# Performance work log

Measured on AMD Instinct MI355X. Metric: run time of the kernel, lower is better.

The kernel has to match this reference:

```python
import jax, jax.numpy as jnp
import numpy as np

D_MODEL = 512
D_STATE = 32
EXPAND = 2
D_INNER = D_MODEL * EXPAND
BATCH = 2
SEQ_LEN = 1024


def setup_inputs() -> dict:
    key = jax.random.key(0)
    ks = jax.random.split(key, 8)
    s = lambda fan_in: 1.0 / np.sqrt(fan_in)
    x = jax.random.normal(ks[0], (BATCH, SEQ_LEN, D_MODEL), dtype=jnp.float32)
    Wx = jax.random.uniform(ks[1], (D_INNER, D_MODEL), minval=-s(D_MODEL), maxval=s(D_MODEL))
    Wdt = jax.random.uniform(ks[2], (D_INNER, D_MODEL), minval=-s(D_MODEL), maxval=s(D_MODEL))
    bdt = jax.random.uniform(ks[3], (D_INNER,)) + 1.0  # dt_proj.bias init: rand + 1
    A_log = jnp.log(jax.random.uniform(ks[4], (D_INNER, D_STATE), minval=1e-4, maxval=1.0))
    WB = jax.random.uniform(ks[5], (D_INNER * D_STATE, D_MODEL), minval=-s(D_MODEL), maxval=s(D_MODEL))
    WC = jax.random.uniform(ks[6], (D_INNER * D_STATE, D_MODEL), minval=-s(D_MODEL), maxval=s(D_MODEL))
    Wout = jax.random.uniform(ks[7], (D_MODEL, D_INNER), minval=-s(D_INNER), maxval=s(D_INNER))
    return {"x": x, "Wx": Wx, "Wdt": Wdt, "bdt": bdt, "A_log": A_log,
            "WB": WB, "WC": WC, "Wout": Wout}


def reference(x, Wx, Wdt, bdt, A_log, WB, WC, Wout):
    b, L, _ = x.shape
    d_inner, d_state = A_log.shape

    x_inner = jnp.einsum('bld,ed->ble', x, Wx)                 # (b, L, d_inner)
    delta = jax.nn.softplus(jnp.einsum('bld,ed->ble', x, Wdt) + bdt)
    A = -jnp.exp(A_log.astype(jnp.float32))                    # (d_inner, d_state)
    A_disc = jnp.exp(delta[..., None] * A)                     # (b, L, d_inner, d_state)
    Bm = jnp.einsum('bld,ed->ble', x, WB).reshape(b, L, d_inner, d_state)
    Cm = jnp.einsum('bld,ed->ble', x, WC).reshape(b, L, d_inner, d_state)

    def step(h, inp):
        a_t, b_t, c_t, x_t = inp
        h = a_t * h + b_t * x_t[..., None]                     # (b, d_inner, d_state)
        y = jnp.sum(c_t * h, axis=-1)                          # (b, d_inner)
        return h, y

    h0 = jnp.zeros((b, d_inner, d_state), dtype=x.dtype)
    xs = (jnp.moveaxis(A_disc, 1, 0), jnp.moveaxis(Bm, 1, 0),
          jnp.moveaxis(Cm, 1, 0), jnp.moveaxis(x_inner, 1, 0))
    _, ys = jax.lax.scan(step, h0, xs)                         # ys: (L, b, d_inner)
    y = jnp.moveaxis(ys, 0, 1)
    y = y * jax.nn.sigmoid(y)                                  # SiLU
    return jnp.einsum('ble,de->bld', y, Wout)
```

## Files before the change

### kernel.cpp

```cpp
#include <hip/hip_runtime.h>

#define BATCH   2
#define SEQLEN  1024
#define DMODEL  512
#define DSTATE  32
#define DINNER  1024
#define MROWS   (BATCH*SEQLEN)
#define NPROJ   (2*DINNER + 2*DINNER*DSTATE)

typedef short bf16x8 __attribute__((ext_vector_type(8)));
typedef float f32x4  __attribute__((ext_vector_type(4)));

__device__ __forceinline__ unsigned short f2bf(float f) {
    union { float f; unsigned u; } c; c.f = f;
    unsigned u = c.u;
    u += 0x7fffu + ((u >> 16) & 1u);
    return (unsigned short)(u >> 16);
}
__device__ __forceinline__ float bf2f(unsigned short h) {
    union { unsigned u; float f; } c; c.u = ((unsigned)h) << 16;
    return c.f;
}

__global__ void cast_all(const float4* __restrict__ Wx, const float4* __restrict__ Wdt,
                         const float4* __restrict__ WB, const float4* __restrict__ WC,
                         const float4* __restrict__ x,  const float4* __restrict__ Wout,
                         unsigned short* __restrict__ Wbf,
                         unsigned short* __restrict__ Xbf,
                         unsigned short* __restrict__ Woutbf) {
    const long nWx = 131072, nWdt = 131072, nWB = 4194304, nWC = 4194304;
    const long nWall = nWx + nWdt + nWB + nWC;
    const long nX = 262144, nWo = 131072;
    const long total = nWall + nX + nWo;
    for (long u = (long)blockIdx.x * blockDim.x + threadIdx.x; u < total;
         u += (long)gridDim.x * blockDim.x) {
        float4 v; unsigned short* dst;
        if (u < nWall) {
            if (u < nWx)             v = Wx[u];
            else if (u < nWx+nWdt)   v = Wdt[u - nWx];
            else if (u < nWx+nWdt+nWB) v = WB[u - nWx - nWdt];
            else                     v = WC[u - nWx - nWdt - nWB];
            dst = Wbf + u*4;
        } else if (u < nWall + nX) {
            v = x[u - nWall];       dst = Xbf + (u - nWall)*4;
        } else {
            v = Wout[u - nWall - nX]; dst = Woutbf + (u - nWall - nX)*4;
        }
        ushort4 o; o.x = f2bf(v.x); o.y = f2bf(v.y); o.z = f2bf(v.z); o.w = f2bf(v.w);
        *(ushort4*)dst = o;
    }
}

template<int EPI>
__global__ __launch_bounds__(256)
void gemm_bt(const unsigned short* __restrict__ A, const unsigned short* __restrict__ Bw,
             int K, int N, int t0, int Tchunk, int tgs,
             float* __restrict__ xin, float* __restrict__ dlt,
             unsigned short* __restrict__ Bout, unsigned short* __restrict__ Cout,
             const float* __restrict__ bdt, float* __restrict__ outf) {
    __shared__ unsigned short Asm[2][128*32];
    __shared__ unsigned short Bsm[2][128*32];
    const int tid  = threadIdx.x;
    const int w    = tid >> 6;
    const int lane = tid & 63;
    const int wm   = w >> 1, wn = w & 1;

    const int nx = gridDim.x, ny = gridDim.y;
    int ntile, rtile;
    if ((nx & 7) == 0) {
        const int lin = blockIdx.x + nx * blockIdx.y;
        const int xcd = lin & 7;
        const int sl  = lin >> 3;
        ntile = xcd * (nx >> 3) + sl / ny;
        rtile = sl % ny;
    } else {
        ntile = blockIdx.x; rtile = blockIdx.y;
    }

    const int rr0  = rtile * 128;
    const int bb   = (rr0 >= Tchunk) ? 1 : 0;
    const int grow0 = bb * SEQLEN + t0 + (rr0 - bb * Tchunk);
    const int n0   = ntile * 128;

    f32x4 acc[4][4] = {};

    const unsigned short* Ag = A  + (size_t)grow0 * K;
    const unsigned short* Bg = Bw + (size_t)n0 * K;

    const int c0 = w*64 + lane;
    const int c1 = c0 + 256;
    const int r   = lane & 15;
    const int h16 = lane >> 4;

    const int rowc0 = c0 >> 2, rowc1 = c1 >> 2;
    const int subc0 = (c0 & 3) ^ ((c0 >> 3) & 3);
    const int subc1 = (c1 & 3) ^ ((c1 >> 3) & 3);
    const size_t srcA0 = (size_t)rowc0 * K + subc0 * 8;
    const size_t srcA1 = (size_t)rowc1 * K + subc1 * 8;

    const int nt = K >> 5;

    #define STAGE(k0_, buf_)                                                              \
        do {                                                                              \
            __builtin_amdgcn_global_load_lds(                                             \
                (const __attribute__((address_space(1))) void*)(Ag + srcA0 + (k0_)),      \
                (__attribute__((address_space(3))) void*)(&Asm[(buf_)][w*512]), 16, 0, 0);\
            __builtin_amdgcn_global_load_lds(                                             \
                (const __attribute__((address_space(1))) void*)(Ag + srcA1 + (k0_)),      \
                (__attribute__((address_space(3))) void*)(&Asm[(buf_)][2048 + w*512]), 16, 0, 0); \
            __builtin_amdgcn_global_load_lds(                                             \
                (const __attribute__((address_space(1))) void*)(Bg + srcA0 + (k0_)),      \
                (__attribute__((address_space(3))) void*)(&Bsm[(buf_)][w*512]), 16, 0, 0);\
            __builtin_amdgcn_global_load_lds(                                             \
                (const __attribute__((address_space(1))) void*)(Bg + srcA1 + (k0_)),      \
                (__attribute__((address_space(3))) void*)(&Bsm[(buf_)][2048 + w*512]), 16, 0, 0); \
        } while (0)

    #define COMPUTE(buf_)                                                                 \
        do {                                                                              \
            bf16x8 af[4], bfr[4];                                                         \
            _Pragma("unroll")                                                             \
            for (int i = 0; i < 4; i++) {                                                 \
                const int Ra = wm*64 + i*16 + r;                                          \
                const int Rb = wn*64 + i*16 + r;                                          \
                af[i]  = *(const bf16x8*)(&Asm[(buf_)][Ra*32 + (h16 ^ ((Ra>>1)&3))*8]);   \
                bfr[i] = *(const bf16x8*)(&Bsm[(buf_)][Rb*32 + (h16 ^ ((Rb>>1)&3))*8]);   \
            }                                                                             \
            _Pragma("unroll")                                                             \
            for (int i = 0; i < 4; i++)                                                   \
                _Pragma("unroll")                                                         \
                for (int j = 0; j < 4; j++)                                               \
                    acc[i][j] = __builtin_amdgcn_mfma_f32_16x16x32_bf16(af[i], bfr[j], acc[i][j], 0, 0, 0); \
        } while (0)

    STAGE(0, 0);
    for (int it = 0; it < nt - 1; ++it) {
        const int cur = it & 1;
        STAGE((it + 1) * 32, cur ^ 1);
        asm volatile("s_waitcnt vmcnt(4)" ::: "memory");
        __builtin_amdgcn_s_barrier();
        COMPUTE(cur);
        asm volatile("" ::: "memory");
        __builtin_amdgcn_s_barrier();
        asm volatile("" ::: "memory");
    }
    asm volatile("s_waitcnt vmcnt(0)" ::: "memory");
    __builtin_amdgcn_s_barrier();
    COMPUTE((nt - 1) & 1);

    #undef STAGE
    #undef COMPUTE

    const int q = lane >> 4;
    const int Tg  = 1 << tgs;
    const int NT  = Tg >> 3;
    #pragma unroll
    for (int i = 0; i < 4; i++) {
        const int lr0 = wm*64 + i*16 + q*4;
        #pragma unroll
        for (int j = 0; j < 4; j++) {
            const int ncol = n0 + wn*64 + j*16 + r;
            if (EPI == 0) {
                const int cr   = rr0 + lr0;
                const int lt   = cr - bb*Tchunk;
                const int seg  = lt >> tgs;
                const int tloc = lt & (Tg - 1);
                const int kin  = tloc >> 3;
                const int tin  = tloc & 7;
                const int bs   = bb*8 + seg;
                if (ncol < 1024) {
                    float4 o = {acc[i][j][0], acc[i][j][1], acc[i][j][2], acc[i][j][3]};
                    *(float4*)(xin + ((size_t)bs*1024 + ncol)*Tg + tloc) = o;
                } else if (ncol < 2048) {
                    const float bias = bdt[ncol - 1024];
                    float4 o;
                    {   float z0 = acc[i][j][0] + bias; o.x = (z0 > 20.f) ? z0 : log1pf(__expf(z0));
                        float z1 = acc[i][j][1] + bias; o.y = (z1 > 20.f) ? z1 : log1pf(__expf(z1));
                        float z2 = acc[i][j][2] + bias; o.z = (z2 > 20.f) ? z2 : log1pf(__expf(z2));
                        float z3 = acc[i][j][3] + bias; o.w = (z3 > 20.f) ? z3 : log1pf(__expf(z3)); }
                    *(float4*)(dlt + ((size_t)bs*1024 + (ncol-1024))*Tg + tloc) = o;
                } else if (ncol < 34816) {
                    const int es = ncol - 2048;
                    short4 o;
                    o.x = (short)f2bf(acc[i][j][0]); o.y = (short)f2bf(acc[i][j][1]);
                    o.z = (short)f2bf(acc[i][j][2]); o.w = (short)f2bf(acc[i][j][3]);
                    *(short4*)(Bout + (((size_t)bs*1024 + (es>>5))*NT + kin)*256 + (es&31)*8 + tin) = o;
                } else {
                    const int es = ncol - 34816;
                    short4 o;
                    o.x = (short)f2bf(acc[i][j][0]); o.y = (short)f2bf(acc[i][j][1]);
                    o.z = (short)f2bf(acc[i][j][2]); o.w = (short)f2bf(acc[i][j][3]);
                    *(short4*)(Cout + (((size_t)bs*1024 + (es>>5))*NT + kin)*256 + (es&31)*8 + tin) = o;
                }
            } else {
                #pragma unroll
                for (int t = 0; t < 4; t++)
                    outf[(size_t)(grow0 + lr0 + t)*N + ncol] = acc[i][j][t];
            }
        }
    }
}

template<int NT>
__global__ __launch_bounds__(256)
void scan_fused(const float* __restrict__ dlt, const float* __restrict__ xin,
                const unsigned short* __restrict__ Bbf, const unsigned short* __restrict__ Cbf,
                const float* __restrict__ A_log,
                unsigned short* __restrict__ Ybf, float* __restrict__ hbuf,
                int t0, int first) {
    const int tid = threadIdx.x;
    const int g = tid >> 5, s = tid & 31;
    const int G = blockIdx.x;
    const int b = G >> 10, e = G & 1023;
    const int bs = b*8 + g;
    const int Tg = NT * 8;

    const float Aes = -__expf(A_log[e*32 + s]);

    const float* dp = dlt + ((size_t)bs*1024 + e)*Tg;
    const float* xp = xin + ((size_t)bs*1024 + e)*Tg;
    const unsigned short* bp = Bbf + ((size_t)bs*1024 + e)*NT*256 + s*8;
    const unsigned short* cp = Cbf + ((size_t)bs*1024 + e)*NT*256 + s*8;

    bf16x8 Bc[NT];
    #pragma unroll
    for (int k = 0; k < NT; k++) Bc[k] = *(const bf16x8*)(bp + (size_t)k*256);

    float h = 0.f, ap = 1.f;
    #pragma unroll
    for (int k = 0; k < NT; k++) {
        const float4 d0 = *(const float4*)(dp + k*8), d1 = *(const float4*)(dp + k*8 + 4);
        const float4 x0 = *(const float4*)(xp + k*8), x1 = *(const float4*)(xp + k*8 + 4);
        const float db[8] = {d0.x,d0.y,d0.z,d0.w,d1.x,d1.y,d1.z,d1.w};
        const float xb[8] = {x0.x,x0.y,x0.z,x0.w,x1.x,x1.y,x1.z,x1.w};
        #pragma unroll
        for (int j = 0; j < 8; j++) {
            const float a = __expf(db[j] * Aes);
            h = a*h + bf2f((unsigned short)Bc[k][j])*xb[j];
            ap *= a;
        }
    }

    __shared__ float Lh[8][32];
    __shared__ float La[8][32];
    Lh[g][s] = h; La[g][s] = ap;
    __syncthreads();
    float hin = first ? 0.f : hbuf[(size_t)G*32 + s];
    #pragma unroll
    for (int j = 0; j < 7; j++) {
        if (j < g) hin = La[j][s]*hin + Lh[j][s];
    }
    if (g == 7) hbuf[(size_t)G*32 + s] = La[7][s]*hin + Lh[7][s];

    h = hin;
    const int tbase = t0 + g*Tg;
    #pragma unroll
    for (int k = 0; k < NT; k++) {
        const bf16x8 cv = *(const bf16x8*)(cp + (size_t)k*256);
        const float4 d0 = *(const float4*)(dp + k*8), d1 = *(const float4*)(dp + k*8 + 4);
        const float4 x0 = *(const float4*)(xp + k*8), x1 = *(const float4*)(xp + k*8 + 4);
        const float db[8] = {d0.x,d0.y,d0.z,d0.w,d1.x,d1.y,d1.z,d1.w};
        const float xb[8] = {x0.x,x0.y,x0.z,x0.w,x1.x,x1.y,x1.z,x1.w};
        float p[8];
        #pragma unroll
        for (int j = 0; j < 8; j++) {
            const float a = __expf(db[j] * Aes);
            h = a*h + bf2f((unsigned short)Bc[k][j])*xb[j];
            p[j] = bf2f((unsigned short)cv[j])*h;
        }
        #pragma unroll
        for (int i2 = 0; i2 < 4; i2++) {
            float send = (s & 16) ? p[i2] : p[i2+4];
            float recv = __shfl_xor(send, 16, 32);
            p[i2] = ((s & 16) ? p[i2+4] : p[i2]) + recv;
        }
        #pragma unroll
        for (int i2 = 0; i2 < 2; i2++) {
            float send = (s & 8) ? p[i2] : p[i2+2];
            float recv = __shfl_xor(send, 8, 32);
            p[i2] = ((s & 8) ? p[i2+2] : p[i2]) + recv;
        }
        {
            float send = (s & 4) ? p[0] : p[1];
            float recv = __shfl_xor(send, 4, 32);
            p[0] = ((s & 4) ? p[1] : p[0]) + recv;
        }
        p[0] += __shfl_xor(p[0], 2, 32);
        p[0] += __shfl_xor(p[0], 1, 32);
        if ((s & 3) == 0) {
            const int tl = s >> 2;
            const float qv = p[0];
            const float y = qv * __builtin_amdgcn_rcpf(1.f + __expf(-qv));
            Ybf[(size_t)b*1048576 + e + (size_t)(tbase + k*8 + tl)*1024] = f2bf(y);
        }
    }
}

extern "C" void kernel_launch(void* const* d_in, const int* in_sizes, int n_in,
                              void* d_out, int out_size, void* d_ws, size_t ws_size,
                              hipStream_t stream) {
    const float* x     = (const float*)d_in[0];
    const float* Wx    = (const float*)d_in[1];
    const float* Wdt   = (const float*)d_in[2];
    const float* bdt   = (const float*)d_in[3];
    const float* A_log = (const float*)d_in[4];
    const float* WB    = (const float*)d_in[5];
    const float* WC    = (const float*)d_in[6];
    const float* Wout  = (const float*)d_in[7];

    char* ws = (char*)d_ws;
    unsigned short* Wbf    = (unsigned short*)(ws);
    unsigned short* Xbf    = (unsigned short*)(ws + 69206016);
    unsigned short* Woutbf = (unsigned short*)(ws + 71303168);
    float*          xin    = (float*)        (ws + 72351744);
    float*          dlt    = (float*)        (ws + 80740352);
    unsigned short* Ybf    = (unsigned short*)(ws + 89128960);
    float*          hbuf   = (float*)        (ws + 93323264);
    unsigned short* Bbf    = (unsigned short*)(ws + 99876864);
    const size_t fixedB = 99876864;

    int T = 128;
    const int cands[4] = {1024, 512, 256, 128};
    for (int ci = 0; ci < 4; ci++) {
        if (fixedB + (size_t)2 * cands[ci] * 131072 <= ws_size) { T = cands[ci]; break; }
    }
    unsigned short* Cbf = Bbf + (size_t)T * 65536;

    const int Tg = T / 8;
    int tgs = 0; while ((1 << tgs) < Tg) tgs++;
    const int NT = Tg / 8;

    cast_all<<<dim3(2048), dim3(256), 0, stream>>>(
        (const float4*)Wx, (const float4*)Wdt, (const float4*)WB, (const float4*)WC,
        (const float4*)x, (const float4*)Wout, Wbf, Xbf, Woutbf);

    const int NC = SEQLEN / T;
    for (int c = 0; c < NC; c++) {
        const int t0 = c * T;
        const int first = (c == 0) ? 1 : 0;
        gemm_bt<0><<<dim3(NPROJ/128, 2*T/128), dim3(256), 0, stream>>>(
            Xbf, Wbf, DMODEL, NPROJ, t0, T, tgs, xin, dlt, Bbf, Cbf, bdt, nullptr);
        if (NT == 16)
            scan_fused<16><<<dim3(2048), dim3(256), 0, stream>>>(
                dlt, xin, Bbf, Cbf, A_log, Ybf, hbuf, t0, first);
        else if (NT == 8)
            scan_fused<8><<<dim3(2048), dim3(256), 0, stream>>>(
                dlt, xin, Bbf, Cbf, A_log, Ybf, hbuf, t0, first);
        else if (NT == 4)
            scan_fused<4><<<dim3(2048), dim3(256), 0, stream>>>(
                dlt, xin, Bbf, Cbf, A_log, Ybf, hbuf, t0, first);
        else
            scan_fused<2><<<dim3(2048), dim3(256), 0, stream>>>(
                dlt, xin, Bbf, Cbf, A_log, Ybf, hbuf, t0, first);
    }

    gemm_bt<1><<<dim3(DMODEL/128, MROWS/128), dim3(256), 0, stream>>>(
        Ybf, Woutbf, DINNER, DMODEL, 0, MROWS, 0, nullptr, nullptr, nullptr, nullptr, nullptr,
        (float*)d_out);
}
```

Baseline: 398.4 us.

## Store x_inner in bf16, reload B per pass, and shrink scan register footprint

The projection epilogue now writes x_inner as bf16 instead of fp32, which halves that intermediate's memory traffic. The scan kernel no longer keeps all B values in registers across both passes. It reloads B in the second pass, uses partial unrolling, and issues the hbuf load early. Workspace offsets shrink, which frees room for larger time chunks and so fewer chunk iterations. The trade-off is lower precision in x_inner and extra B reads in exchange for lower register pressure.

```diff
diff --git a/kernel.cpp b/kernel.cpp
--- a/kernel.cpp
+++ b/kernel.cpp
@@ -55,7 +55,7 @@
 __global__ __launch_bounds__(256)
 void gemm_bt(const unsigned short* __restrict__ A, const unsigned short* __restrict__ Bw,
              int K, int N, int t0, int Tchunk, int tgs,
-             float* __restrict__ xin, float* __restrict__ dlt,
+             unsigned short* __restrict__ xinb, float* __restrict__ dlt,
              unsigned short* __restrict__ Bout, unsigned short* __restrict__ Cout,
              const float* __restrict__ bdt, float* __restrict__ outf) {
     __shared__ unsigned short Asm[2][128*32];
@@ -169,8 +169,10 @@
                 const int tin  = tloc & 7;
                 const int bs   = bb*8 + seg;
                 if (ncol < 1024) {
-                    float4 o = {acc[i][j][0], acc[i][j][1], acc[i][j][2], acc[i][j][3]};
-                    *(float4*)(xin + ((size_t)bs*1024 + ncol)*Tg + tloc) = o;
+                    short4 o;
+                    o.x = (short)f2bf(acc[i][j][0]); o.y = (short)f2bf(acc[i][j][1]);
+                    o.z = (short)f2bf(acc[i][j][2]); o.w = (short)f2bf(acc[i][j][3]);
+                    *(short4*)(xinb + ((size_t)bs*1024 + ncol)*Tg + tloc) = o;
                 } else if (ncol < 2048) {
                     const float bias = bdt[ncol - 1024];
                     float4 o;
@@ -203,7 +205,7 @@
 
 template<int NT>
 __global__ __launch_bounds__(256)
-void scan_fused(const float* __restrict__ dlt, const float* __restrict__ xin,
+void scan_fused(const float* __restrict__ dlt, const unsigned short* __restrict__ xinb,
                 const unsigned short* __restrict__ Bbf, const unsigned short* __restrict__ Cbf,
                 const float* __restrict__ A_log,
                 unsigned short* __restrict__ Ybf, float* __restrict__ hbuf,
@@ -217,26 +219,24 @@
 
     const float Aes = -__expf(A_log[e*32 + s]);
 
-    const float* dp = dlt + ((size_t)bs*1024 + e)*Tg;
-    const float* xp = xin + ((size_t)bs*1024 + e)*Tg;
-    const unsigned short* bp = Bbf + ((size_t)bs*1024 + e)*NT*256 + s*8;
-    const unsigned short* cp = Cbf + ((size_t)bs*1024 + e)*NT*256 + s*8;
-
-    bf16x8 Bc[NT];
-    #pragma unroll
-    for (int k = 0; k < NT; k++) Bc[k] = *(const bf16x8*)(bp + (size_t)k*256);
+    const float*          dp = dlt  + ((size_t)bs*1024 + e)*Tg;
+    const unsigned short* xp = xinb + ((size_t)bs*1024 + e)*Tg;
+    const unsigned short* bp = Bbf  + ((size_t)bs*1024 + e)*NT*256 + s*8;
+    const unsigned short* cp = Cbf  + ((size_t)bs*1024 + e)*NT*256 + s*8;
+
+    const float hin0 = first ? 0.f : hbuf[(size_t)G*32 + s];
 
     float h = 0.f, ap = 1.f;
-    #pragma unroll
+    #pragma unroll 2
     for (int k = 0; k < NT; k++) {
+        const bf16x8 bv = *(const bf16x8*)(bp + (size_t)k*256);
+        const bf16x8 xv = *(const bf16x8*)(xp + k*8);
         const float4 d0 = *(const float4*)(dp + k*8), d1 = *(const float4*)(dp + k*8 + 4);
-        const float4 x0 = *(const float4*)(xp + k*8), x1 = *(const float4*)(xp + k*8 + 4);
         const float db[8] = {d0.x,d0.y,d0.z,d0.w,d1.x,d1.y,d1.z,d1.w};
-        const float xb[8] = {x0.x,x0.y,x0.z,x0.w,x1.x,x1.y,x1.z,x1.w};
         #pragma unroll
         for (int j = 0; j < 8; j++) {
             const float a = __expf(db[j] * Aes);
-            h = a*h + bf2f((unsigned short)Bc[k][j])*xb[j];
+            h = a*h + bf2f((unsigned short)bv[j])*bf2f((unsigned short)xv[j]);
             ap *= a;
         }
     }
@@ -245,7 +245,7 @@
     __shared__ float La[8][32];
     Lh[g][s] = h; La[g][s] = ap;
     __syncthreads();
-    float hin = first ? 0.f : hbuf[(size_t)G*32 + s];
+    float hin = hin0;
     #pragma unroll
     for (int j = 0; j < 7; j++) {
         if (j < g) hin = La[j][s]*hin + Lh[j][s];
@@ -254,18 +254,18 @@
 
     h = hin;
     const int tbase = t0 + g*Tg;
-    #pragma unroll
+    #pragma unroll 2
     for (int k = 0; k < NT; k++) {
+        const bf16x8 bv = *(const bf16x8*)(bp + (size_t)k*256);
         const bf16x8 cv = *(const bf16x8*)(cp + (size_t)k*256);
+        const bf16x8 xv = *(const bf16x8*)(xp + k*8);
         const float4 d0 = *(const float4*)(dp + k*8), d1 = *(const float4*)(dp + k*8 + 4);
-        const float4 x0 = *(const float4*)(xp + k*8), x1 = *(const float4*)(xp + k*8 + 4);
         const float db[8] = {d0.x,d0.y,d0.z,d0.w,d1.x,d1.y,d1.z,d1.w};
-        const float xb[8] = {x0.x,x0.y,x0.z,x0.w,x1.x,x1.y,x1.z,x1.w};
         float p[8];
         #pragma unroll
         for (int j = 0; j < 8; j++) {
             const float a = __expf(db[j] * Aes);
-            h = a*h + bf2f((unsigned short)Bc[k][j])*xb[j];
+            h = a*h + bf2f((unsigned short)bv[j])*bf2f((unsigned short)xv[j]);
             p[j] = bf2f((unsigned short)cv[j])*h;
         }
         #pragma unroll
@@ -312,12 +312,12 @@
     unsigned short* Wbf    = (unsigned short*)(ws);
     unsigned short* Xbf    = (unsigned short*)(ws + 69206016);
     unsigned short* Woutbf = (unsigned short*)(ws + 71303168);
-    float*          xin    = (float*)        (ws + 72351744);
-    float*          dlt    = (float*)        (ws + 80740352);
-    unsigned short* Ybf    = (unsigned short*)(ws + 89128960);
-    float*          hbuf   = (float*)        (ws + 93323264);
-    unsigned short* Bbf    = (unsigned short*)(ws + 99876864);
-    const size_t fixedB = 99876864;
+    unsigned short* xinb   = (unsigned short*)(ws + 72351744);
+    float*          dlt    = (float*)        (ws + 76546048);
+    unsigned short* Ybf    = (unsigned short*)(ws + 84934656);
+    float*          hbuf   = (float*)        (ws + 89128960);
+    unsigned short* Bbf    = (unsigned short*)(ws + 89391104);
+    const size_t fixedB = 89391104;
 
     int T = 128;
     const int cands[4] = {1024, 512, 256, 128};
@@ -339,19 +339,19 @@
         const int t0 = c * T;
         const int first = (c == 0) ? 1 : 0;
         gemm_bt<0><<<dim3(NPROJ/128, 2*T/128), dim3(256), 0, stream>>>(
-            Xbf, Wbf, DMODEL, NPROJ, t0, T, tgs, xin, dlt, Bbf, Cbf, bdt, nullptr);
+            Xbf, Wbf, DMODEL, NPROJ, t0, T, tgs, xinb, dlt, Bbf, Cbf, bdt, nullptr);
         if (NT == 16)
             scan_fused<16><<<dim3(2048), dim3(256), 0, stream>>>(
-                dlt, xin, Bbf, Cbf, A_log, Ybf, hbuf, t0, first);
+                dlt, xinb, Bbf, Cbf, A_log, Ybf, hbuf, t0, first);
         else if (NT == 8)
             scan_fused<8><<<dim3(2048), dim3(256), 0, stream>>>(
-                dlt, xin, Bbf, Cbf, A_log, Ybf, hbuf, t0, first);
+                dlt, xinb, Bbf, Cbf, A_log, Ybf, hbuf, t0, first);
         else if (NT == 4)
             scan_fused<4><<<dim3(2048), dim3(256), 0, stream>>>(
-                dlt, xin, Bbf, Cbf, A_log, Ybf, hbuf, t0, first);
+                dlt, xinb, Bbf, Cbf, A_log, Ybf, hbuf, t0, first);
         else
             scan_fused<2><<<dim3(2048), dim3(256), 0, stream>>>(
-                dlt, xin, Bbf, Cbf, A_log, Ybf, hbuf, t0, first);
+                dlt, xinb, Bbf, Cbf, A_log, Ybf, hbuf, t0, first);
     }
 
     gemm_bt<1><<<dim3(DMODEL/128, MROWS/128), dim3(256), 0, stream>>>(
```

Result: no change. 396.4 us (-0.5%).
